# Performance work log

Measured on AMD Instinct MI355X. Metric: run time of the kernel, lower is better.

The kernel has to match this reference:

```python
import jax, jax.numpy as jnp
import numpy as np

B, R, H = 64, 32, 1024  # batch, num_rounds, lstm_hidden_size
IN = 2 * H              # GatedTrans in_dim
EPS = 1e-12             # F.normalize eps


def _gated(x, Wy, by, Wg, bg):
    # GatedTrans: tanh branch * leaky_relu branch (slope 0.01, torch default)
    return jnp.tanh(x @ Wy + by) * jax.nn.leaky_relu(x @ Wg + bg, 0.01)


def setup_inputs() -> dict:
    key = jax.random.key(0)
    ks = jax.random.split(key, 12)
    s_in = 1.0 / np.sqrt(IN)
    s_h = 1.0 / np.sqrt(H)
    return {
        "hist": jax.random.normal(ks[0], (B, R, IN), jnp.float32),
        "ques": jax.random.normal(ks[1], (B, R, IN), jnp.float32),
        "W_hy": jax.random.normal(ks[2], (IN, H), jnp.float32) * s_in,
        "b_hy": jnp.zeros((H,), jnp.float32),
        "W_hg": jax.random.normal(ks[3], (IN, H), jnp.float32) * s_in,
        "b_hg": jnp.zeros((H,), jnp.float32),
        "W_qy": jax.random.normal(ks[4], (IN, H), jnp.float32) * s_in,
        "b_qy": jnp.zeros((H,), jnp.float32),
        "W_qg": jax.random.normal(ks[5], (IN, H), jnp.float32) * s_in,
        "b_qg": jnp.zeros((H,), jnp.float32),
        "W_att": jax.random.normal(ks[6], (H,), jnp.float32) * s_h,
        "b_att": jnp.zeros((), jnp.float32),
    }


def reference(hist, ques, W_hy, b_hy, W_hg, b_hg, W_qy, b_qy, W_qg, b_qg, W_att, b_att):
    hist_embed = _gated(hist, W_hy, b_hy, W_hg, b_hg)   # [B, R, H]
    ques_embed = _gated(ques, W_qy, b_qy, W_qg, b_qg)   # [B, R, H]
    # broadcast outer product over rounds: [B, Rq, Rh, H]
    att_embed = ques_embed[:, :, None, :] * hist_embed[:, None, :, :]
    norm = jnp.sqrt(jnp.sum(att_embed * att_embed, axis=-1, keepdims=True))
    att_embed = att_embed / jnp.maximum(norm, EPS)       # F.normalize(p=2)
    scores = att_embed @ W_att + b_att                   # [B, Rq, Rh]
    att = jax.nn.softmax(scores, axis=-1)
    tril = jnp.tril(jnp.ones((R, R), jnp.float32))       # causal round mask
    att_masked = att * tril
    att_masked = att_masked / jnp.sum(att_masked, axis=-1, keepdims=True)
    # weighted sum over hist rounds: [B, Rq, 2H]
    feat = jnp.einsum("bqh,bhd->bqd", att_masked, hist)
    return feat
```

## Files before the change

kernel.cpp:

```cpp
#include <hip/hip_runtime.h>
#include <cstdint>

#define IN_DIM 2048
#define H_DIM  1024
#define BROWS  2048
#define BATCH  64
#define ROUNDS 32

typedef __bf16 bf16x8 __attribute__((ext_vector_type(8)));
typedef float  f32x4  __attribute__((ext_vector_type(4)));
typedef unsigned short u16;

__device__ __forceinline__ u16 f2bf(float f) {
    unsigned int u = __float_as_uint(f);
    u += 0x7FFFu + ((u >> 16) & 1u);
    return (u16)(u >> 16);
}

__device__ __forceinline__ void async_ld16(const void* g, void* l) {
    __builtin_amdgcn_global_load_lds(
        (__attribute__((address_space(1))) void*)(uintptr_t)g,
        (__attribute__((address_space(3))) void*)(unsigned int)(uintptr_t)l,
        16, 0, 0);
}

__global__ __launch_bounds__(256) void prep(
    const float* __restrict__ hist, const float* __restrict__ ques,
    u16* __restrict__ xh, u16* __restrict__ xq,
    const float* __restrict__ why, const float* __restrict__ whg,
    const float* __restrict__ wqy, const float* __restrict__ wqg,
    u16* __restrict__ oh, u16* __restrict__ oq)
{
    int idx = blockIdx.x;
    if (idx < 4096) {
        int i = idx * 256 + threadIdx.x;
        const float4* h4 = (const float4*)hist;
        const float4* q4 = (const float4*)ques;
        float4 a = h4[i], b = q4[i];
        ushort4 oa, ob;
        oa.x = f2bf(a.x); oa.y = f2bf(a.y); oa.z = f2bf(a.z); oa.w = f2bf(a.w);
        ob.x = f2bf(b.x); ob.y = f2bf(b.y); ob.z = f2bf(b.z); ob.w = f2bf(b.w);
        ((ushort4*)xh)[i] = oa;
        ((ushort4*)xq)[i] = ob;
        return;
    }
    __shared__ float t[64][35];
    int zz = idx - 4096;
    int z = zz >> 11, rem = zz & 2047;
    const float* Y = z == 0 ? why : wqy;
    const float* G = z == 0 ? whg : wqg;
    u16* O = z == 0 ? oh : oq;
    int n0 = (rem & 63) * 32;
    int k0 = (rem >> 6) * 64;
    int hc0 = n0 >> 1;
    int tx = threadIdx.x & 31, ty = threadIdx.x >> 5;
    const float* S = (tx < 16) ? Y : G;
    int sc = hc0 + (tx & 15);
    #pragma unroll
    for (int r = 0; r < 8; r++)
        t[ty + 8 * r][tx] = S[(size_t)(k0 + ty + 8 * r) * H_DIM + sc];
    __syncthreads();
    int ln = threadIdx.x >> 3, lg = threadIdx.x & 7;
    u16 vals[8];
    #pragma unroll
    for (int j = 0; j < 8; j++) vals[j] = f2bf(t[lg * 8 + j][ln]);
    *(uint4*)&O[(size_t)(n0 + ln) * IN_DIM + k0 + lg * 8] = *(const uint4*)vals;
}

__global__ __launch_bounds__(256) void gemm_act(
    const u16* __restrict__ xh, const u16* __restrict__ xq,
    const u16* __restrict__ wth, const u16* __restrict__ wtq,
    const float* __restrict__ bhy, const float* __restrict__ bhg,
    const float* __restrict__ bqy, const float* __restrict__ bqg,
    u16* __restrict__ eh, u16* __restrict__ eq)
{
    int L = blockIdx.x;
    int cluster = L & 7;
    int slot = L >> 3;
    int z  = cluster >> 2;
    int y  = (cluster & 1) * 8 + (slot >> 3);
    int x  = ((cluster >> 1) & 1) * 8 + (slot & 7);
    int m0 = y * 128, n0 = x * 128;

    const u16* A  = z == 0 ? xh : xq;
    const u16* Bt = z == 0 ? wth : wtq;
    const float* by = z == 0 ? bhy : bqy;
    const float* bg = z == 0 ? bhg : bqg;
    u16* E = z == 0 ? eh : eq;

    __shared__ __align__(16) u16 As[2][128 * 64];
    __shared__ __align__(16) u16 Bs[2][128 * 64];

    int tid = threadIdx.x;
    int wave = tid >> 6, lane = tid & 63;
    int lane15 = lane & 15, quad = lane >> 4;
    int wm = (wave >> 1) * 64, wn = (wave & 1) * 64;

    f32x4 acc[4][4];
    #pragma unroll
    for (int i = 0; i < 4; i++)
        #pragma unroll
        for (int j = 0; j < 4; j++) acc[i][j] = (f32x4){0.f, 0.f, 0.f, 0.f};

    int srow[4], skc[4], scb[4];
    #pragma unroll
    for (int r2 = 0; r2 < 4; r2++) {
        int cbase = r2 * 256 + wave * 64;
        int cs = cbase + lane;
        int row = cs >> 3, s = cs & 7;
        srow[r2] = row; skc[r2] = s ^ (row & 7); scb[r2] = cbase;
    }

    #define STAGE(buf, kt)                                                                   \
        _Pragma("unroll")                                                                    \
        for (int r2 = 0; r2 < 4; r2++) {                                                     \
            async_ld16(A  + (size_t)(m0 + srow[r2]) * IN_DIM + (kt) + skc[r2] * 8,           \
                       &As[buf][scb[r2] * 8]);                                               \
            async_ld16(Bt + (size_t)(n0 + srow[r2]) * IN_DIM + (kt) + skc[r2] * 8,           \
                       &Bs[buf][scb[r2] * 8]);                                               \
        }

    #define COMPUTE(buf)                                                                     \
        _Pragma("unroll")                                                                    \
        for (int ks = 0; ks < 2; ks++) {                                                     \
            bf16x8 af[4], bfv[4];                                                            \
            _Pragma("unroll")                                                                \
            for (int i = 0; i < 4; i++) {                                                    \
                int row = wm + i * 16 + lane15;                                              \
                int s = (ks * 4 + quad) ^ (row & 7);                                         \
                af[i] = *(const bf16x8*)&As[buf][row * 64 + s * 8];                          \
            }                                                                                \
            _Pragma("unroll")                                                                \
            for (int j = 0; j < 4; j++) {                                                    \
                int row = wn + j * 16 + lane15;                                              \
                int s = (ks * 4 + quad) ^ (row & 7);                                         \
                bfv[j] = *(const bf16x8*)&Bs[buf][row * 64 + s * 8];                         \
            }                                                                                \
            _Pragma("unroll")                                                                \
            for (int i = 0; i < 4; i++)                                                      \
                _Pragma("unroll")                                                            \
                for (int j = 0; j < 4; j++)                                                  \
                    acc[i][j] = __builtin_amdgcn_mfma_f32_16x16x32_bf16(                     \
                        af[i], bfv[j], acc[i][j], 0, 0, 0);                                  \
        }

    STAGE(0, 0)
    for (int kt = 0; kt < IN_DIM; kt += 128) {
        __syncthreads();
        STAGE(1, kt + 64)
        COMPUTE(0)
        __syncthreads();
        if (kt + 128 < IN_DIM) STAGE(0, kt + 128)
        COMPUTE(1)
    }
    #undef STAGE
    #undef COMPUTE

    int n0w = n0 + wn;
    #pragma unroll
    for (int jp = 0; jp < 2; jp++) {
        int hc = (n0w >> 1) + jp * 16 + lane15;
        float vy = by[hc], vg = bg[hc];
        #pragma unroll
        for (int i = 0; i < 4; i++) {
            #pragma unroll
            for (int r = 0; r < 4; r++) {
                int row = m0 + wm + i * 16 + quad * 4 + r;
                float y2 = tanhf(acc[i][2 * jp][r] + vy);
                float g = acc[i][2 * jp + 1][r] + vg;
                E[(size_t)row * H_DIM + hc] = f2bf(y2 * (g > 0.f ? g : 0.01f * g));
            }
        }
    }
}

__global__ __launch_bounds__(256) void score_feat(
    const u16* __restrict__ eh, const u16* __restrict__ eq,
    const float* __restrict__ hist, const float* __restrict__ watt,
    const float* __restrict__ batt, float* __restrict__ out)
{
    int idx = blockIdx.x;
    int b = idx & 63, q = idx >> 6;
    int tid = threadIdx.x, wave = tid >> 6, lane = tid & 63;
    __shared__ float sw[32], swn[32];

    const u16* qe = eq + (size_t)(b * ROUNDS + q) * H_DIM;
    float uw[16], u2[16];
    #pragma unroll
    for (int c = 0; c < 2; c++) {
        uint4 pk = ((const uint4*)qe)[lane + 64 * c];
        float4 w0 = ((const float4*)watt)[(lane + 64 * c) * 2];
        float4 w1 = ((const float4*)watt)[(lane + 64 * c) * 2 + 1];
        unsigned int ws[4] = {pk.x, pk.y, pk.z, pk.w};
        float wf[8] = {w0.x, w0.y, w0.z, w0.w, w1.x, w1.y, w1.z, w1.w};
        #pragma unroll
        for (int e = 0; e < 4; e++) {
            float lo = __uint_as_float(ws[e] << 16);
            float hi = __uint_as_float(ws[e] & 0xFFFF0000u);
            uw[c * 8 + 2 * e]     = lo * wf[2 * e];
            u2[c * 8 + 2 * e]     = lo * lo;
            uw[c * 8 + 2 * e + 1] = hi * wf[2 * e + 1];
            u2[c * 8 + 2 * e + 1] = hi * hi;
        }
    }
    for (int h = wave; h <= q; h += 4) {
        const u16* he = eh + (size_t)(b * ROUNDS + h) * H_DIM;
        float num = 0.f, nrm = 0.f;
        #pragma unroll
        for (int c = 0; c < 2; c++) {
            uint4 pk = ((const uint4*)he)[lane + 64 * c];
            unsigned int vs[4] = {pk.x, pk.y, pk.z, pk.w};
            #pragma unroll
            for (int e = 0; e < 4; e++) {
                float lo = __uint_as_float(vs[e] << 16);
                float hi = __uint_as_float(vs[e] & 0xFFFF0000u);
                num += uw[c * 8 + 2 * e] * lo + uw[c * 8 + 2 * e + 1] * hi;
                nrm += u2[c * 8 + 2 * e] * lo * lo + u2[c * 8 + 2 * e + 1] * hi * hi;
            }
        }
        #pragma unroll
        for (int off = 32; off > 0; off >>= 1) {
            num += __shfl_down(num, off);
            nrm += __shfl_down(nrm, off);
        }
        if (lane == 0)
            sw[h] = num / fmaxf(sqrtf(nrm), 1e-12f) + batt[0];
    }
    __syncthreads();
    if (tid == 0) {
        float mx = -1e30f;
        for (int h = 0; h <= q; h++) mx = fmaxf(mx, sw[h]);
        float zs = 0.f;
        for (int h = 0; h <= q; h++) { float e = expf(sw[h] - mx); swn[h] = e; zs += e; }
        float inv = 1.f / zs;
        for (int h = 0; h <= q; h++) swn[h] *= inv;
    }
    __syncthreads();
    const float4* hb = (const float4*)(hist + (size_t)b * ROUNDS * IN_DIM);
    float4* ob = (float4*)(out + (size_t)(b * ROUNDS + q) * IN_DIM);
    #pragma unroll
    for (int d0 = 0; d0 < 2; d0++) {
        int d = tid + d0 * 256;
        float4 a = {0.f, 0.f, 0.f, 0.f};
        for (int h = 0; h <= q; h++) {
            float w = swn[h];
            float4 x = hb[h * 512 + d];
            a.x += w * x.x; a.y += w * x.y; a.z += w * x.z; a.w += w * x.w;
        }
        ob[d] = a;
    }
}

extern "C" void kernel_launch(void* const* d_in, const int* in_sizes, int n_in,
                              void* d_out, int out_size, void* d_ws, size_t ws_size,
                              hipStream_t stream) {
    const float* hist = (const float*)d_in[0];
    const float* ques = (const float*)d_in[1];
    const float* Why  = (const float*)d_in[2];
    const float* bhy  = (const float*)d_in[3];
    const float* Whg  = (const float*)d_in[4];
    const float* bhg  = (const float*)d_in[5];
    const float* Wqy  = (const float*)d_in[6];
    const float* bqy  = (const float*)d_in[7];
    const float* Wqg  = (const float*)d_in[8];
    const float* bqg  = (const float*)d_in[9];
    const float* watt = (const float*)d_in[10];
    const float* batt = (const float*)d_in[11];
    float* out = (float*)d_out;

    char* w = (char*)d_ws;
    u16* Xh  = (u16*)w;
    u16* Xq  = Xh  + (size_t)BROWS * IN_DIM;
    u16* WtH = Xq  + (size_t)BROWS * IN_DIM;
    u16* WtQ = WtH + (size_t)IN_DIM * IN_DIM;
    u16* Eh  = WtQ + (size_t)IN_DIM * IN_DIM;
    u16* Eq  = Eh  + (size_t)BROWS * H_DIM;

    prep<<<8192, 256, 0, stream>>>(hist, ques, Xh, Xq, Why, Whg, Wqy, Wqg, WtH, WtQ);
    gemm_act<<<512, 256, 0, stream>>>(Xh, Xq, WtH, WtQ, bhy, bhg, bqy, bqg, Eh, Eq);
    score_feat<<<2048, 256, 0, stream>>>(Eh, Eq, hist, watt, batt, out);
}
```

Measured before the change: 186.9 us.

## Switch gated GEMM from bf16 to scaled FP8 e4m3 MFMA

Inputs and weights are converted to FP8 e4m3 with a ×16 prescale instead of bf16, and the GEMM uses the MX-scaled 16x16x128 f8f6f4 MFMA with a fixed exponent scale compensating the prescale. The K tile doubles to 128 bytes per row, which halves the number of loop iterations, and memory traffic for the operands halves. This trades numerical precision for more MFMA throughput and less bandwidth, with a risk of accuracy loss against the fp32 reference.

```diff
diff --git a/kernel.cpp b/kernel.cpp
--- a/kernel.cpp
+++ b/kernel.cpp
@@ -1,4 +1,5 @@
 #include <hip/hip_runtime.h>
+#include <hip/hip_fp8.h>
 #include <cstdint>
 
 #define IN_DIM 2048
@@ -7,14 +8,20 @@
 #define BATCH  64
 #define ROUNDS 32
 
-typedef __bf16 bf16x8 __attribute__((ext_vector_type(8)));
-typedef float  f32x4  __attribute__((ext_vector_type(4)));
+typedef float f32x4 __attribute__((ext_vector_type(4)));
+typedef int   v8i   __attribute__((ext_vector_type(8)));
+typedef int   v4i   __attribute__((ext_vector_type(4)));
 typedef unsigned short u16;
+typedef unsigned char  u8;
 
 __device__ __forceinline__ u16 f2bf(float f) {
     unsigned int u = __float_as_uint(f);
     u += 0x7FFFu + ((u >> 16) & 1u);
     return (u16)(u >> 16);
+}
+__device__ __forceinline__ u8 f2fp8(float f) {
+    __hip_fp8_e4m3 v(f);
+    return v.__x;
 }
 
 __device__ __forceinline__ void async_ld16(const void* g, void* l) {
@@ -26,10 +33,10 @@
 
 __global__ __launch_bounds__(256) void prep(
     const float* __restrict__ hist, const float* __restrict__ ques,
-    u16* __restrict__ xh, u16* __restrict__ xq,
+    u8* __restrict__ xh, u8* __restrict__ xq,
     const float* __restrict__ why, const float* __restrict__ whg,
     const float* __restrict__ wqy, const float* __restrict__ wqg,
-    u16* __restrict__ oh, u16* __restrict__ oq)
+    u8* __restrict__ oh, u8* __restrict__ oq)
 {
     int idx = blockIdx.x;
     if (idx < 4096) {
@@ -37,11 +44,16 @@
         const float4* h4 = (const float4*)hist;
         const float4* q4 = (const float4*)ques;
         float4 a = h4[i], b = q4[i];
-        ushort4 oa, ob;
-        oa.x = f2bf(a.x); oa.y = f2bf(a.y); oa.z = f2bf(a.z); oa.w = f2bf(a.w);
-        ob.x = f2bf(b.x); ob.y = f2bf(b.y); ob.z = f2bf(b.z); ob.w = f2bf(b.w);
-        ((ushort4*)xh)[i] = oa;
-        ((ushort4*)xq)[i] = ob;
+        unsigned int pa = (unsigned int)f2fp8(16.f * a.x) |
+                          ((unsigned int)f2fp8(16.f * a.y) << 8) |
+                          ((unsigned int)f2fp8(16.f * a.z) << 16) |
+                          ((unsigned int)f2fp8(16.f * a.w) << 24);
+        unsigned int pb = (unsigned int)f2fp8(16.f * b.x) |
+                          ((unsigned int)f2fp8(16.f * b.y) << 8) |
+                          ((unsigned int)f2fp8(16.f * b.z) << 16) |
+                          ((unsigned int)f2fp8(16.f * b.w) << 24);
+        ((unsigned int*)xh)[i] = pa;
+        ((unsigned int*)xq)[i] = pb;
         return;
     }
     __shared__ float t[64][35];
@@ -49,27 +61,26 @@
     int z = zz >> 11, rem = zz & 2047;
     const float* Y = z == 0 ? why : wqy;
     const float* G = z == 0 ? whg : wqg;
-    u16* O = z == 0 ? oh : oq;
+    u8* O = z == 0 ? oh : oq;
     int n0 = (rem & 63) * 32;
     int k0 = (rem >> 6) * 64;
-    int hc0 = n0 >> 1;
     int tx = threadIdx.x & 31, ty = threadIdx.x >> 5;
     const float* S = (tx < 16) ? Y : G;
-    int sc = hc0 + (tx & 15);
+    int sc = (n0 >> 1) + (tx & 15);
     #pragma unroll
     for (int r = 0; r < 8; r++)
         t[ty + 8 * r][tx] = S[(size_t)(k0 + ty + 8 * r) * H_DIM + sc];
     __syncthreads();
     int ln = threadIdx.x >> 3, lg = threadIdx.x & 7;
-    u16 vals[8];
-    #pragma unroll
-    for (int j = 0; j < 8; j++) vals[j] = f2bf(t[lg * 8 + j][ln]);
-    *(uint4*)&O[(size_t)(n0 + ln) * IN_DIM + k0 + lg * 8] = *(const uint4*)vals;
+    u8 vals[8];
+    #pragma unroll
+    for (int j = 0; j < 8; j++) vals[j] = f2fp8(16.f * t[lg * 8 + j][ln]);
+    *(uint2*)&O[(size_t)(n0 + ln) * IN_DIM + k0 + lg * 8] = *(const uint2*)vals;
 }
 
 __global__ __launch_bounds__(256) void gemm_act(
-    const u16* __restrict__ xh, const u16* __restrict__ xq,
-    const u16* __restrict__ wth, const u16* __restrict__ wtq,
+    const u8* __restrict__ xh, const u8* __restrict__ xq,
+    const u8* __restrict__ wth, const u8* __restrict__ wtq,
     const float* __restrict__ bhy, const float* __restrict__ bhg,
     const float* __restrict__ bqy, const float* __restrict__ bqg,
     u16* __restrict__ eh, u16* __restrict__ eq)
@@ -82,14 +93,14 @@
     int x  = ((cluster >> 1) & 1) * 8 + (slot & 7);
     int m0 = y * 128, n0 = x * 128;
 
-    const u16* A  = z == 0 ? xh : xq;
-    const u16* Bt = z == 0 ? wth : wtq;
+    const u8* A  = z == 0 ? xh : xq;
+    const u8* Bt = z == 0 ? wth : wtq;
     const float* by = z == 0 ? bhy : bqy;
     const float* bg = z == 0 ? bhg : bqg;
     u16* E = z == 0 ? eh : eq;
 
-    __shared__ __align__(16) u16 As[2][128 * 64];
-    __shared__ __align__(16) u16 Bs[2][128 * 64];
+    __shared__ __align__(16) u8 As[2][128 * 128];
+    __shared__ __align__(16) u8 Bs[2][128 * 128];
 
     int tid = threadIdx.x;
     int wave = tid >> 6, lane = tid & 63;
@@ -114,46 +125,49 @@
     #define STAGE(buf, kt)                                                                   \
         _Pragma("unroll")                                                                    \
         for (int r2 = 0; r2 < 4; r2++) {                                                     \
-            async_ld16(A  + (size_t)(m0 + srow[r2]) * IN_DIM + (kt) + skc[r2] * 8,           \
-                       &As[buf][scb[r2] * 8]);                                               \
-            async_ld16(Bt + (size_t)(n0 + srow[r2]) * IN_DIM + (kt) + skc[r2] * 8,           \
-                       &Bs[buf][scb[r2] * 8]);                                               \
+            async_ld16(A  + (size_t)(m0 + srow[r2]) * IN_DIM + (kt) + skc[r2] * 16,          \
+                       &As[buf][scb[r2] * 16]);                                              \
+            async_ld16(Bt + (size_t)(n0 + srow[r2]) * IN_DIM + (kt) + skc[r2] * 16,          \
+                       &Bs[buf][scb[r2] * 16]);                                              \
+        }
+
+    #define LOADFRAG(dst, base, row)                                                         \
+        {                                                                                    \
+            int p0 = ((quad * 2)     ^ ((row) & 7)) * 16;                                    \
+            int p1 = ((quad * 2 + 1) ^ ((row) & 7)) * 16;                                    \
+            v4i lo = *(const v4i*)&(base)[(row) * 128 + p0];                                 \
+            v4i hi = *(const v4i*)&(base)[(row) * 128 + p1];                                 \
+            dst[0] = lo[0]; dst[1] = lo[1]; dst[2] = lo[2]; dst[3] = lo[3];                  \
+            dst[4] = hi[0]; dst[5] = hi[1]; dst[6] = hi[2]; dst[7] = hi[3];                  \
         }
 
     #define COMPUTE(buf)                                                                     \
-        _Pragma("unroll")                                                                    \
-        for (int ks = 0; ks < 2; ks++) {                                                     \
-            bf16x8 af[4], bfv[4];                                                            \
+        {                                                                                    \
+            v8i af[4], bfv[4];                                                               \
             _Pragma("unroll")                                                                \
-            for (int i = 0; i < 4; i++) {                                                    \
-                int row = wm + i * 16 + lane15;                                              \
-                int s = (ks * 4 + quad) ^ (row & 7);                                         \
-                af[i] = *(const bf16x8*)&As[buf][row * 64 + s * 8];                          \
-            }                                                                                \
+            for (int i = 0; i < 4; i++) LOADFRAG(af[i], As[buf], (wm + i * 16 + lane15))     \
             _Pragma("unroll")                                                                \
-            for (int j = 0; j < 4; j++) {                                                    \
-                int row = wn + j * 16 + lane15;                                              \
-                int s = (ks * 4 + quad) ^ (row & 7);                                         \
-                bfv[j] = *(const bf16x8*)&Bs[buf][row * 64 + s * 8];                         \
-            }                                                                                \
+            for (int j = 0; j < 4; j++) LOADFRAG(bfv[j], Bs[buf], (wn + j * 16 + lane15))    \
             _Pragma("unroll")                                                                \
             for (int i = 0; i < 4; i++)                                                      \
                 _Pragma("unroll")                                                            \
                 for (int j = 0; j < 4; j++)                                                  \
-                    acc[i][j] = __builtin_amdgcn_mfma_f32_16x16x32_bf16(                     \
-                        af[i], bfv[j], acc[i][j], 0, 0, 0);                                  \
+                    acc[i][j] = __builtin_amdgcn_mfma_scale_f32_16x16x128_f8f6f4(            \
+                        af[i], bfv[j], acc[i][j], 0, 0,                                      \
+                        0, 0x7B7B7B7B, 0, 0x7B7B7B7B);                                       \
         }
 
     STAGE(0, 0)
-    for (int kt = 0; kt < IN_DIM; kt += 128) {
+    for (int kt = 0; kt < IN_DIM; kt += 256) {
         __syncthreads();
-        STAGE(1, kt + 64)
+        STAGE(1, kt + 128)
         COMPUTE(0)
         __syncthreads();
-        if (kt + 128 < IN_DIM) STAGE(0, kt + 128)
+        if (kt + 256 < IN_DIM) STAGE(0, kt + 256)
         COMPUTE(1)
     }
     #undef STAGE
+    #undef LOADFRAG
     #undef COMPUTE
 
     int n0w = n0 + wn;
@@ -269,12 +283,12 @@
     float* out = (float*)d_out;
 
     char* w = (char*)d_ws;
-    u16* Xh  = (u16*)w;
-    u16* Xq  = Xh  + (size_t)BROWS * IN_DIM;
-    u16* WtH = Xq  + (size_t)BROWS * IN_DIM;
-    u16* WtQ = WtH + (size_t)IN_DIM * IN_DIM;
-    u16* Eh  = WtQ + (size_t)IN_DIM * IN_DIM;
-    u16* Eq  = Eh  + (size_t)BROWS * H_DIM;
+    u8* Xh   = (u8*)w;
+    u8* Xq   = Xh  + (size_t)BROWS * IN_DIM;
+    u8* WtH  = Xq  + (size_t)BROWS * IN_DIM;
+    u8* WtQ  = WtH + (size_t)IN_DIM * IN_DIM;
+    u16* Eh  = (u16*)(WtQ + (size_t)IN_DIM * IN_DIM);
+    u16* Eq  = Eh + (size_t)BROWS * H_DIM;
 
     prep<<<8192, 256, 0, stream>>>(hist, ques, Xh, Xq, Why, Whg, Wqy, Wqg, WtH, WtQ);
     gemm_act<<<512, 256, 0, stream>>>(Xh, Xq, WtH, WtQ, bhy, bhg, bqy, bqg, Eh, Eq);
```

Result: slower. 319.6 us (+71.0%).
